# Optimization experiments

Hardware: AMD Instinct MI355X
Metric: run time of the kernel (lower is better)

## Reference

```python
import jax, jax.numpy as jnp
import numpy as np

EPS = 1e-5  # torch BatchNorm1d default eps

def _bn_train(h, gamma, beta):
    # BatchNorm1d in training mode on [B, C] (L=1 after global pool):
    # stats over the batch axis, biased variance.
    mu = h.mean(axis=0)
    var = ((h - mu) ** 2).mean(axis=0)
    return (h - mu) * jax.lax.rsqrt(var + EPS) * gamma + beta

def setup_inputs() -> dict:
    key = jax.random.key(0)
    k_x, k_w1, k_w2 = jax.random.split(key, 3)
    B, C, L = 16, 256, 16384
    Cr = C // 2  # reduction = 2
    x = jax.random.normal(k_x, (B, C, L), dtype=jnp.float32)
    # Conv1d kernel_size=1, bias=False -> channel matmuls; kaiming-ish scale
    w1 = jax.random.normal(k_w1, (Cr, C), dtype=jnp.float32) * (1.0 / np.sqrt(C))
    w2 = jax.random.normal(k_w2, (C, Cr), dtype=jnp.float32) * (1.0 / np.sqrt(Cr))
    g1 = jnp.ones((Cr,), jnp.float32)
    b1 = jnp.zeros((Cr,), jnp.float32)
    g2 = jnp.ones((C,), jnp.float32)
    b2 = jnp.zeros((C,), jnp.float32)
    return {"x": x, "w1": w1, "g1": g1, "b1": b1, "w2": w2, "g2": g2, "b2": b2}

def reference(x, w1, g1, b1, w2, g2, b2):
    # x: [B, C, L]
    s = x.mean(axis=-1)                      # AdaptiveAvgPool1d(1) -> [B, C]
    h = jnp.einsum('bc,rc->br', s, w1)       # 1x1 conv squeeze -> [B, Cr]
    h = _bn_train(h, g1, b1)
    h = jax.nn.gelu(h, approximate=False)    # torch nn.GELU default (erf)
    h = jnp.einsum('br,cr->bc', h, w2)       # 1x1 conv excite -> [B, C]
    h = _bn_train(h, g2, b2)
    gate = jax.nn.sigmoid(h)                 # [B, C]
    return x * gate[:, :, None]              # broadcast multiply over L
```

## Files before the change

kernel.cpp:

```cpp
#include <hip/hip_runtime.h>
#include <math.h>

#define B 16
#define C 256
#define CR 128
#define L 16384
#define NROW (B * C)
#define THREADS 256
#define ITERS (L / 4 / THREADS)

__global__ __launch_bounds__(THREADS) void row_mean_kernel(
    const float* __restrict__ x, float* __restrict__ s) {
    const int row = blockIdx.x;
    const int t = threadIdx.x;
    const float4* xr = (const float4*)(x + (size_t)row * L);

    float acc = 0.0f;
#pragma unroll
    for (int i = 0; i < ITERS; ++i) {
        float4 v = xr[t + i * THREADS];
        acc += (v.x + v.y) + (v.z + v.w);
    }
#pragma unroll
    for (int off = 32; off > 0; off >>= 1) acc += __shfl_down(acc, off, 64);

    __shared__ float wsum[THREADS / 64];
    if ((t & 63) == 0) wsum[t >> 6] = acc;
    __syncthreads();
    if (t == 0) {
        float tot = 0.0f;
#pragma unroll
        for (int w = 0; w < THREADS / 64; ++w) tot += wsum[w];
        s[row] = tot * (1.0f / (float)L);
    }
}

__global__ __launch_bounds__(THREADS) void se_mlp_kernel(
    const float* __restrict__ s_in,
    const float* __restrict__ w1, const float* __restrict__ g1, const float* __restrict__ b1,
    const float* __restrict__ w2, const float* __restrict__ g2, const float* __restrict__ b2,
    float* __restrict__ gate) {
    __shared__ float s[B * C];
    __shared__ float h1[B * CR];
    __shared__ float h2[B * C];
    const int t = threadIdx.x;

    for (int i = t; i < B * C; i += THREADS) s[i] = s_in[i];
    __syncthreads();

    for (int i = t; i < B * CR; i += THREADS) {
        const int b = i / CR, r = i % CR;
        const float* sv = &s[b * C];
        const float* wv = &w1[r * C];
        float acc = 0.0f;
#pragma unroll 4
        for (int c = 0; c < C; ++c) acc = fmaf(sv[c], wv[c], acc);
        h1[i] = acc;
    }
    __syncthreads();

    if (t < CR) {
        float mu = 0.0f;
#pragma unroll
        for (int b = 0; b < B; ++b) mu += h1[b * CR + t];
        mu *= (1.0f / (float)B);
        float var = 0.0f;
#pragma unroll
        for (int b = 0; b < B; ++b) {
            float d = h1[b * CR + t] - mu;
            var = fmaf(d, d, var);
        }
        var *= (1.0f / (float)B);
        const float inv = rsqrtf(var + 1e-5f);
        const float gg = g1[t], bb = b1[t];
#pragma unroll
        for (int b = 0; b < B; ++b) {
            float v = (h1[b * CR + t] - mu) * inv * gg + bb;
            v = 0.5f * v * (1.0f + erff(v * 0.70710678118654752440f));
            h1[b * CR + t] = v;
        }
    }
    __syncthreads();

    for (int i = t; i < B * C; i += THREADS) {
        const int b = i / C, c = i % C;
        const float* gv = &h1[b * CR];
        const float* wv = &w2[c * CR];
        float acc = 0.0f;
#pragma unroll 4
        for (int r = 0; r < CR; ++r) acc = fmaf(gv[r], wv[r], acc);
        h2[i] = acc;
    }
    __syncthreads();

    {
        float mu = 0.0f;
#pragma unroll
        for (int b = 0; b < B; ++b) mu += h2[b * C + t];
        mu *= (1.0f / (float)B);
        float var = 0.0f;
#pragma unroll
        for (int b = 0; b < B; ++b) {
            float d = h2[b * C + t] - mu;
            var = fmaf(d, d, var);
        }
        var *= (1.0f / (float)B);
        const float inv = rsqrtf(var + 1e-5f);
        const float gg = g2[t], bb = b2[t];
#pragma unroll
        for (int b = 0; b < B; ++b) {
            float v = (h2[b * C + t] - mu) * inv * gg + bb;
            gate[b * C + t] = 1.0f / (1.0f + expf(-v));
        }
    }
}

__global__ __launch_bounds__(THREADS) void scale_kernel(
    const float* __restrict__ x, const float* __restrict__ gate,
    float* __restrict__ out) {
    const int row = blockIdx.x;
    const int t = threadIdx.x;
    const float g = gate[row];
    const float4* xr = (const float4*)(x + (size_t)row * L);
    float4* orow = (float4*)(out + (size_t)row * L);
#pragma unroll
    for (int i = 0; i < ITERS; ++i) {
        float4 v = xr[t + i * THREADS];
        v.x *= g; v.y *= g; v.z *= g; v.w *= g;
        orow[t + i * THREADS] = v;
    }
}

extern "C" void kernel_launch(void* const* d_in, const int* in_sizes, int n_in,
                              void* d_out, int out_size, void* d_ws, size_t ws_size,
                              hipStream_t stream) {
    const float* x  = (const float*)d_in[0];
    const float* w1 = (const float*)d_in[1];
    const float* g1 = (const float*)d_in[2];
    const float* b1 = (const float*)d_in[3];
    const float* w2 = (const float*)d_in[4];
    const float* g2 = (const float*)d_in[5];
    const float* b2 = (const float*)d_in[6];
    float* out = (float*)d_out;

    float* s    = (float*)d_ws;
    float* gate = s + NROW;

    row_mean_kernel<<<NROW, THREADS, 0, stream>>>(x, s);
    se_mlp_kernel<<<1, THREADS, 0, stream>>>(s, w1, g1, b1, w2, g2, b2, gate);
    scale_kernel<<<NROW, THREADS, 0, stream>>>(x, gate, out);
}
```

Before: 626.3 us.

## Split single-block SE MLP into two multi-block kernels parallel over output channels

Replaces the one-block MLP kernel with two kernels: one block per squeeze channel for the first matmul plus BatchNorm and GELU, and one block per output channel for the second matmul plus BatchNorm and sigmoid. Each block computes the 16 batch dot products with float4 loads and sub-wavefront shuffle reductions, then does the batch statistics in shared memory. This removes the serial bottleneck of a single block doing all the MLP work, at the cost of one extra kernel launch and a global round trip for the hidden activations.

```diff
diff --git a/kernel.cpp b/kernel.cpp
--- a/kernel.cpp
+++ b/kernel.cpp
@@ -35,83 +35,84 @@
     }
 }
 
-__global__ __launch_bounds__(THREADS) void se_mlp_kernel(
-    const float* __restrict__ s_in,
-    const float* __restrict__ w1, const float* __restrict__ g1, const float* __restrict__ b1,
-    const float* __restrict__ w2, const float* __restrict__ g2, const float* __restrict__ b2,
-    float* __restrict__ gate) {
-    __shared__ float s[B * C];
-    __shared__ float h1[B * CR];
-    __shared__ float h2[B * C];
+__global__ __launch_bounds__(256) void mlp1_kernel(
+    const float* __restrict__ s, const float* __restrict__ w1,
+    const float* __restrict__ g1, const float* __restrict__ b1,
+    float* __restrict__ h1) {
+    const int r = blockIdx.x;
     const int t = threadIdx.x;
+    const int b = t >> 4;
+    const int j = t & 15;
 
-    for (int i = t; i < B * C; i += THREADS) s[i] = s_in[i];
+    const float4* sv = (const float4*)(s + b * C) + j * 4;
+    const float4* wv = (const float4*)(w1 + r * C) + j * 4;
+    float acc = 0.0f;
+#pragma unroll
+    for (int k = 0; k < 4; ++k) {
+        float4 a = sv[k], w = wv[k];
+        acc += a.x * w.x + a.y * w.y + a.z * w.z + a.w * w.w;
+    }
+#pragma unroll
+    for (int off = 8; off > 0; off >>= 1) acc += __shfl_down(acc, off, 16);
+
+    __shared__ float h[B];
+    if (j == 0) h[b] = acc;
     __syncthreads();
 
-    for (int i = t; i < B * CR; i += THREADS) {
-        const int b = i / CR, r = i % CR;
-        const float* sv = &s[b * C];
-        const float* wv = &w1[r * C];
-        float acc = 0.0f;
-#pragma unroll 4
-        for (int c = 0; c < C; ++c) acc = fmaf(sv[c], wv[c], acc);
-        h1[i] = acc;
+    float mu = 0.0f;
+#pragma unroll
+    for (int i = 0; i < B; ++i) mu += h[i];
+    mu *= (1.0f / (float)B);
+    float var = 0.0f;
+#pragma unroll
+    for (int i = 0; i < B; ++i) { float d = h[i] - mu; var = fmaf(d, d, var); }
+    var *= (1.0f / (float)B);
+    const float inv = rsqrtf(var + 1e-5f);
+
+    if (t < B) {
+        float v = (h[t] - mu) * inv * g1[r] + b1[r];
+        v = 0.5f * v * (1.0f + erff(v * 0.70710678118654752440f));
+        h1[t * CR + r] = v;
     }
+}
+
+__global__ __launch_bounds__(128) void mlp2_kernel(
+    const float* __restrict__ h1, const float* __restrict__ w2,
+    const float* __restrict__ g2, const float* __restrict__ b2,
+    float* __restrict__ gate) {
+    const int c = blockIdx.x;
+    const int t = threadIdx.x;
+    const int b = t >> 3;
+    const int j = t & 7;
+
+    const float4* hv = (const float4*)(h1 + b * CR) + j * 4;
+    const float4* wv = (const float4*)(w2 + c * CR) + j * 4;
+    float acc = 0.0f;
+#pragma unroll
+    for (int k = 0; k < 4; ++k) {
+        float4 a = hv[k], w = wv[k];
+        acc += a.x * w.x + a.y * w.y + a.z * w.z + a.w * w.w;
+    }
+#pragma unroll
+    for (int off = 4; off > 0; off >>= 1) acc += __shfl_down(acc, off, 8);
+
+    __shared__ float h[B];
+    if (j == 0) h[b] = acc;
     __syncthreads();
 
-    if (t < CR) {
-        float mu = 0.0f;
+    float mu = 0.0f;
 #pragma unroll
-        for (int b = 0; b < B; ++b) mu += h1[b * CR + t];
-        mu *= (1.0f / (float)B);
-        float var = 0.0f;
+    for (int i = 0; i < B; ++i) mu += h[i];
+    mu *= (1.0f / (float)B);
+    float var = 0.0f;
 #pragma unroll
-        for (int b = 0; b < B; ++b) {
-            float d = h1[b * CR + t] - mu;
-            var = fmaf(d, d, var);
-        }
-        var *= (1.0f / (float)B);
-        const float inv = rsqrtf(var + 1e-5f);
-        const float gg = g1[t], bb = b1[t];
-#pragma unroll
-        for (int b = 0; b < B; ++b) {
-            float v = (h1[b * CR + t] - mu) * inv * gg + bb;
-            v = 0.5f * v * (1.0f + erff(v * 0.70710678118654752440f));
-            h1[b * CR + t] = v;
-        }
-    }
-    __syncthreads();
+    for (int i = 0; i < B; ++i) { float d = h[i] - mu; var = fmaf(d, d, var); }
+    var *= (1.0f / (float)B);
+    const float inv = rsqrtf(var + 1e-5f);
 
-    for (int i = t; i < B * C; i += THREADS) {
-        const int b = i / C, c = i % C;
-        const float* gv = &h1[b * CR];
-        const float* wv = &w2[c * CR];
-        float acc = 0.0f;
-#pragma unroll 4
-        for (int r = 0; r < CR; ++r) acc = fmaf(gv[r], wv[r], acc);
-        h2[i] = acc;
-    }
-    __syncthreads();
-
-    {
-        float mu = 0.0f;
-#pragma unroll
-        for (int b = 0; b < B; ++b) mu += h2[b * C + t];
-        mu *= (1.0f / (float)B);
-        float var = 0.0f;
-#pragma unroll
-        for (int b = 0; b < B; ++b) {
-            float d = h2[b * C + t] - mu;
-            var = fmaf(d, d, var);
-        }
-        var *= (1.0f / (float)B);
-        const float inv = rsqrtf(var + 1e-5f);
-        const float gg = g2[t], bb = b2[t];
-#pragma unroll
-        for (int b = 0; b < B; ++b) {
-            float v = (h2[b * C + t] - mu) * inv * gg + bb;
-            gate[b * C + t] = 1.0f / (1.0f + expf(-v));
-        }
+    if (t < B) {
+        float v = (h[t] - mu) * inv * g2[c] + b2[c];
+        gate[t * C + c] = 1.0f / (1.0f + expf(-v));
     }
 }
 
@@ -144,9 +145,11 @@
     float* out = (float*)d_out;
 
     float* s    = (float*)d_ws;
-    float* gate = s + NROW;
+    float* h1   = s + NROW;
+    float* gate = h1 + B * CR;
 
     row_mean_kernel<<<NROW, THREADS, 0, stream>>>(x, s);
-    se_mlp_kernel<<<1, THREADS, 0, stream>>>(s, w1, g1, b1, w2, g2, b2, gate);
+    mlp1_kernel<<<CR, 256, 0, stream>>>(s, w1, g1, b1, h1);
+    mlp2_kernel<<<C, 128, 0, stream>>>(h1, w2, g2, b2, gate);
     scale_kernel<<<NROW, THREADS, 0, stream>>>(x, gate, out);
 }
```

Measured after the change: 505.6 us. -19.3%, faster.
